# Optimization experiments

Measured on AMD Instinct MI355X. Metric: run time of the kernel, lower is better.

Reference implementation:

```python
import math
import jax, jax.numpy as jnp
import numpy as np

D_MODEL = 1024
N_HEADS = 16
D_K = D_MODEL // N_HEADS


def _alibi_slopes(n_heads):
    # Faithful to the torch _get_slopes: slopes[i] = 2**(-8 + i), subsampled if
    # n_heads is not a power of two.
    power = 2 ** math.ceil(math.log2(n_heads))
    slopes = np.array([2.0 ** (-8 + i) for i in range(power)], dtype=np.float32)
    if n_heads != power:
        ratio = power // n_heads
        slopes = slopes[np.arange(0, power, ratio)][:n_heads]
    return jnp.asarray(slopes)


def setup_inputs() -> dict:
    key = jax.random.key(0)
    ks = jax.random.split(key, 11)
    B, S, D = 2, 2048, D_MODEL
    w = 0.02  # weight init scale
    return {
        "query": jax.random.normal(ks[0], (B, S, D), jnp.float32),
        "key": jax.random.normal(ks[1], (B, S, D), jnp.float32),
        "value": jax.random.normal(ks[2], (B, S, D), jnp.float32),
        "Wq": jax.random.normal(ks[3], (D, D), jnp.float32) * w,
        "bq": jax.random.normal(ks[4], (D,), jnp.float32) * w,
        "Wk": jax.random.normal(ks[5], (D, D), jnp.float32) * w,
        "bk": jax.random.normal(ks[6], (D,), jnp.float32) * w,
        "Wv": jax.random.normal(ks[7], (D, D), jnp.float32) * w,
        "bv": jax.random.normal(ks[8], (D,), jnp.float32) * w,
        "Wo": jax.random.normal(ks[9], (D, D), jnp.float32) * w,
        "bo": jax.random.normal(ks[10], (D,), jnp.float32) * w,
    }


def reference(query, key, value, Wq, bq, Wk, bk, Wv, bv, Wo, bo):
    B, Sq, D = query.shape
    Sk = key.shape[1]
    H, dk = N_HEADS, D_K

    # projections (torch Linear: x @ W.T + b)
    q = (query @ Wq.T + bq).reshape(B, Sq, H, dk).transpose(0, 2, 1, 3)  # [B,H,Sq,dk]
    k = (key @ Wk.T + bk).reshape(B, Sk, H, dk).transpose(0, 2, 1, 3)    # [B,H,Sk,dk]
    v = (value @ Wv.T + bv).reshape(B, Sk, H, dk).transpose(0, 2, 1, 3)  # [B,H,Sk,dk]

    scores = jnp.einsum("bhqd,bhkd->bhqk", q, k) / jnp.sqrt(jnp.float32(dk))

    # ALiBi bias: slopes[h] * (i - j), non-causal path (is_causal=False)
    dist = (jnp.arange(Sq)[:, None] - jnp.arange(Sk)[None, :]).astype(scores.dtype)
    slopes = _alibi_slopes(H)
    scores = scores + slopes[None, :, None, None] * dist[None, None, :, :]

    attn = jax.nn.softmax(scores, axis=-1)
    out = jnp.einsum("bhqk,bhkd->bhqd", attn, v)          # [B,H,Sq,dk]
    out = out.transpose(0, 2, 1, 3).reshape(B, Sq, D)     # [B,Sq,D]
    return out @ Wo.T + bo
```

## Files before the change

### kernel.cpp

```cpp
#include <hip/hip_runtime.h>

typedef __bf16 bf16_t;
typedef bf16_t bf16x8 __attribute__((ext_vector_type(8)));
typedef float f32x4 __attribute__((ext_vector_type(4)));
typedef float f32x16 __attribute__((ext_vector_type(16)));
typedef unsigned short u16x4 __attribute__((ext_vector_type(4)));
typedef unsigned int u32x4v __attribute__((ext_vector_type(4)));
typedef unsigned int u32;

#define DEV static __device__ __forceinline__


DEV unsigned short f2bf(float f) {
  unsigned int u = __builtin_bit_cast(unsigned int, f);
  u = (u + 0x7fffu + ((u >> 16) & 1u)) >> 16;
  return (unsigned short)u;
}

DEV float fexp2(float x) {
  float r;
  asm("v_exp_f32 %0, %1" : "=v"(r) : "v"(x));
  return r;
}

DEV u32 cvtpk(float lo, float hi_) {
  u32 r;
  asm("v_cvt_pk_bf16_f32 %0, %1, %2" : "=v"(r) : "v"(lo), "v"(hi_));
  return r;
}

DEV void plswap(u32& a, u32& b) {
  asm("v_permlane32_swap_b32 %0, %1" : "+v"(a), "+v"(b));
}

DEV void async_ld16(const unsigned short* gsrc, unsigned short* lbase, int lane) {
#if __has_builtin(__builtin_amdgcn_global_load_lds)
  __builtin_amdgcn_global_load_lds(
      (const __attribute__((address_space(1))) unsigned int*)(const void*)gsrc,
      (__attribute__((address_space(3))) unsigned int*)(void*)lbase, 16, 0, 0);
#else
  *reinterpret_cast<u32x4v*>(reinterpret_cast<char*>(lbase) + lane * 16) =
      *reinterpret_cast<const u32x4v*>(gsrc);
#endif
}


DEV void cvt_body(const float* __restrict__ src, unsigned short* __restrict__ dst, int i) {
  const float4* s = reinterpret_cast<const float4*>(src) + (size_t)i * 2;
  float4 a = s[0], c = s[1];
  u16x4 lo = {f2bf(a.x), f2bf(a.y), f2bf(a.z), f2bf(a.w)};
  u16x4 hi = {f2bf(c.x), f2bf(c.y), f2bf(c.z), f2bf(c.w)};
  u16x4* d = reinterpret_cast<u16x4*>(dst) + (size_t)i * 2;
  d[0] = lo;
  d[1] = hi;
}

__global__ __launch_bounds__(256) void cvt_all(
    const float* __restrict__ q, const float* __restrict__ k, const float* __restrict__ v,
    const float* __restrict__ Wq, const float* __restrict__ Wk, const float* __restrict__ Wv,
    const float* __restrict__ Wo, unsigned short* dq, unsigned short* dk, unsigned short* dv,
    unsigned short* dWq, unsigned short* dWk, unsigned short* dWv, unsigned short* dWo) {
  const int bid = blockIdx.x;
  const float* src;
  unsigned short* dst;
  int i;
  if (bid < 6144) {
    const int z = bid >> 11;
    src = z == 0 ? q : z == 1 ? k : v;
    dst = z == 0 ? dq : z == 1 ? dk : dv;
    i = (bid & 2047) * 256 + threadIdx.x;
  } else {
    const int z = (bid - 6144) >> 9;
    src = z == 0 ? Wq : z == 1 ? Wk : z == 2 ? Wv : Wo;
    dst = z == 0 ? dWq : z == 1 ? dWk : z == 2 ? dWv : dWo;
    i = ((bid - 6144) & 511) * 256 + threadIdx.x;
  }
  cvt_body(src, dst, i);
}


DEV void stage_a128(const unsigned short* __restrict__ G, int row0, int k0,
                    unsigned short* lbuf, int lane, int wv) {
#pragma unroll
  for (int r = 0; r < 4; ++r) {
    const int rowA = (r * 4 + wv) * 8 + (lane >> 3);
    const int chunk = (lane & 7) ^ (rowA & 7);
    async_ld16(G + (size_t)(row0 + rowA) * 1024 + k0 + chunk * 8, lbuf + (r * 4 + wv) * 512,
               lane);
  }
}

DEV void stage_b64(const unsigned short* __restrict__ G, int row0, int k0,
                   unsigned short* lbuf, int lane, int wv) {
#pragma unroll
  for (int r = 0; r < 2; ++r) {
    const int rowB = (r * 4 + wv) * 8 + (lane >> 3);
    const int chunk = (lane & 7) ^ (rowB & 7);
    async_ld16(G + (size_t)(row0 + rowB) * 1024 + k0 + chunk * 8, lbuf + (r * 4 + wv) * 512,
               lane);
  }
}

DEV void gemm_core(const unsigned short* __restrict__ X, const unsigned short* __restrict__ W,
                   unsigned short* lA0, unsigned short* lA1, unsigned short* lB0,
                   unsigned short* lB1, int bm0, int bn0, int lane, int wv, int wm, int wn,
                   f32x4 acc[4][2]) {
  stage_a128(X, bm0, 0, lA0, lane, wv);
  stage_b64(W, bn0, 0, lB0, lane, wv);
  __syncthreads();
  for (int kt = 0; kt < 16; ++kt) {
    unsigned short* lA = (kt & 1) ? lA1 : lA0;
    unsigned short* lB = (kt & 1) ? lB1 : lB0;
    unsigned short* nA = (kt & 1) ? lA0 : lA1;
    unsigned short* nB = (kt & 1) ? lB0 : lB1;
    if (kt < 15) {
      stage_a128(X, bm0, (kt + 1) * 64, nA, lane, wv);
      stage_b64(W, bn0, (kt + 1) * 64, nB, lane, wv);
    }
#pragma unroll
    for (int kk = 0; kk < 2; ++kk) {
      bf16x8 af[4], bfr[2];
#pragma unroll
      for (int f = 0; f < 4; ++f) {
        const int rowA = wm * 64 + f * 16 + (lane & 15);
        const int cA = (kk * 4 + (lane >> 4)) ^ (rowA & 7);
        af[f] = *reinterpret_cast<const bf16x8*>(lA + rowA * 64 + cA * 8);
      }
#pragma unroll
      for (int f = 0; f < 2; ++f) {
        const int rowB = wn * 32 + f * 16 + (lane & 15);
        const int cB = (kk * 4 + (lane >> 4)) ^ (rowB & 7);
        bfr[f] = *reinterpret_cast<const bf16x8*>(lB + rowB * 64 + cB * 8);
      }
#pragma unroll
      for (int i = 0; i < 4; ++i)
#pragma unroll
        for (int j = 0; j < 2; ++j)
          acc[i][j] = __builtin_amdgcn_mfma_f32_16x16x32_bf16(af[i], bfr[j], acc[i][j], 0, 0, 0);
    }
    __syncthreads();
  }
}


__global__ __launch_bounds__(256, 3) void gemm_qkv_kernel(
    const unsigned short* __restrict__ Xq, const unsigned short* __restrict__ Xk,
    const unsigned short* __restrict__ Xv, const unsigned short* __restrict__ Wq,
    const unsigned short* __restrict__ Wk, const unsigned short* __restrict__ Wv,
    const float* __restrict__ bq, const float* __restrict__ bk, const float* __restrict__ bv,
    unsigned short* __restrict__ Qp, unsigned short* __restrict__ Kp,
    unsigned short* __restrict__ Vp, unsigned* __restrict__ nb2) {
  __shared__ unsigned short lA[2][8192];
  __shared__ unsigned short lB[2][4096];
  const int flat = blockIdx.x + 32 * blockIdx.y + 512 * blockIdx.z;
  const int swz = (flat & 7) * 192 + (flat >> 3);
  const int bx = swz & 31;
  const int by = (swz >> 5) & 15;
  const int bz = swz >> 9;
  const unsigned short* X;
  const unsigned short* W;
  const float* bias;
  unsigned short* dst;
  if (bz == 0) { X = Xq; W = Wq; bias = bq; dst = Qp; }
  else if (bz == 1) { X = Xk; W = Wk; bias = bk; dst = Kp; }
  else { X = Xv; W = Wv; bias = bv; dst = Vp; }
  const bool zV = (bz == 2);
  const bool zK = (bz == 1) && (nb2 != nullptr);
  const int lane = threadIdx.x & 63, wv = threadIdx.x >> 6;
  const int wm = wv >> 1, wn = wv & 1;
  const int bm0 = bx * 128, bn0 = by * 64;
  f32x4 acc[4][2] = {};
  gemm_core(X, W, lA[0], lA[1], lB[0], lB[1], bm0, bn0, lane, wv, wm, wn, acc);
  float rowmax = 0.0f;
#pragma unroll
  for (int i = 0; i < 4; ++i) {
    const int mbase = bm0 + wm * 64 + i * 16 + ((lane >> 4) << 2);
#pragma unroll
    for (int r = 0; r < 4; ++r) {
      const int m = mbase + r;
      const int b = m >> 11, s = m & 2047;
      float ssp = 0.0f;
#pragma unroll
      for (int j = 0; j < 2; ++j) {
        const int n = bn0 + wn * 32 + j * 16 + (lane & 15);
        const float val = acc[i][j][r] + bias[n];
        const unsigned short v16 = f2bf(val);
        const int h = n >> 6, d = n & 63;
        if (zV)
          dst[((size_t)(b * 16 + h) * 64 + d) * 2048 + s] = v16;
        else
          dst[((size_t)(b * 16 + h) * 2048 + s) * 64 + d] = v16;
        ssp = __builtin_fmaf(val, val, ssp);
      }
      if (zK) {
        ssp += __shfl_xor(ssp, 1);
        ssp += __shfl_xor(ssp, 2);
        ssp += __shfl_xor(ssp, 4);
        ssp += __shfl_xor(ssp, 8);
        rowmax = fmaxf(rowmax, ssp);
      }
    }
  }
  if (zK) {
    rowmax = fmaxf(rowmax, __shfl_xor(rowmax, 16));
    rowmax = fmaxf(rowmax, __shfl_xor(rowmax, 32));
    if (lane == 0)
      atomicMax(nb2 + (((bm0 >> 11) * 16 + by) * 2 + wn), __float_as_uint(rowmax));
  }
}


__global__ __launch_bounds__(256, 3) void gemm_out_kernel(const unsigned short* __restrict__ X,
                                                          const unsigned short* __restrict__ W,
                                                          const float* __restrict__ bias,
                                                          float* __restrict__ out) {
  __shared__ unsigned short lA[2][8192];
  __shared__ unsigned short lB[2][4096];
  const int flat = blockIdx.x + 32 * blockIdx.y;
  const int swz = (flat & 7) * 64 + (flat >> 3);
  const int bx = swz & 31, by = swz >> 5;
  const int lane = threadIdx.x & 63, wv = threadIdx.x >> 6;
  const int wm = wv >> 1, wn = wv & 1;
  const int bm0 = bx * 128, bn0 = by * 64;
  f32x4 acc[4][2] = {};
  gemm_core(X, W, lA[0], lA[1], lB[0], lB[1], bm0, bn0, lane, wv, wm, wn, acc);
#pragma unroll
  for (int i = 0; i < 4; ++i) {
    const int mbase = bm0 + wm * 64 + i * 16 + ((lane >> 4) << 2);
#pragma unroll
    for (int j = 0; j < 2; ++j) {
      const int n = bn0 + wn * 32 + j * 16 + (lane & 15);
      const float bia = bias[n];
#pragma unroll
      for (int r = 0; r < 4; ++r) out[(size_t)(mbase + r) * 1024 + n] = acc[i][j][r] + bia;
    }
  }
}


__global__ __launch_bounds__(256) void knorm_kernel(const unsigned short* __restrict__ Kp,
                                                    unsigned* __restrict__ nb2) {
  const int bh = blockIdx.y;
  const int s = blockIdx.x * 256 + threadIdx.x;
  const u32x4v* row = reinterpret_cast<const u32x4v*>(Kp + ((size_t)bh * 2048 + s) * 64);
  float ss0 = 0.0f, ss1 = 0.0f;
#pragma unroll
  for (int c = 0; c < 8; ++c) {
    u32x4v u = row[c];
    float acc = 0.0f;
#pragma unroll
    for (int e = 0; e < 4; ++e) {
      const float lo = __builtin_bit_cast(float, u[e] << 16);
      const float hi = __builtin_bit_cast(float, u[e] & 0xFFFF0000u);
      acc = __builtin_fmaf(lo, lo, acc);
      acc = __builtin_fmaf(hi, hi, acc);
    }
    if (c < 4) ss0 += acc;
    else ss1 += acc;
  }
#pragma unroll
  for (int off = 1; off <= 32; off <<= 1) {
    ss0 = fmaxf(ss0, __shfl_xor(ss0, off));
    ss1 = fmaxf(ss1, __shfl_xor(ss1, off));
  }
  if ((threadIdx.x & 63) == 0) {
    atomicMax(nb2 + bh * 2, __float_as_uint(ss0));
    atomicMax(nb2 + bh * 2 + 1, __float_as_uint(ss1));
  }
}


__global__ __launch_bounds__(128) void attn_prepass(const unsigned short* __restrict__ Qp,
                                                    const unsigned short* __restrict__ Kp,
                                                    const unsigned* __restrict__ nb2,
                                                    float* __restrict__ mfA,
                                                    float* __restrict__ bltA) {
  __shared__ float sred[4];
  const int lane = threadIdx.x & 63, wv = threadIdx.x >> 6;
  const int lq = lane & 31, hi = lane >> 5;
  const int qt = blockIdx.x, bh = blockIdx.y, h = bh & 15;
  const float L2E = 1.4426950408889634f;
  const float slope2 = ldexpf(L2E, h - 8);
  const float SC2 = 0.125f * L2E;
  const size_t headoff = (size_t)bh * 2048 * 64;
  const unsigned short* Qh = Qp + headoff;
  const unsigned short* Kh = Kp + headoff;
  const int q_glob = qt * 64 + wv * 32 + lq;

  bf16x8 qf[4];
#pragma unroll
  for (int tt = 0; tt < 4; ++tt)
    qf[tt] = *reinterpret_cast<const bf16x8*>(Qh + (size_t)q_glob * 64 + tt * 16 + hi * 8);

  float qq = 0.0f;
#pragma unroll
  for (int tt = 0; tt < 4; ++tt)
#pragma unroll
    for (int e = 0; e < 8; ++e) {
      const float x = (float)qf[tt][e];
      qq = __builtin_fmaf(x, x, qq);
    }
  qq += __shfl_xor(qq, 32);
#pragma unroll
  for (int off = 1; off <= 16; off <<= 1) qq = fmaxf(qq, __shfl_xor(qq, off));

  f32x16 s0 = {}, s1 = {};
#pragma unroll
  for (int tt = 0; tt < 4; ++tt) {
    bf16x8 k0 = *reinterpret_cast<const bf16x8*>(Kh + (size_t)lq * 64 + tt * 16 + hi * 8);
    s0 = __builtin_amdgcn_mfma_f32_32x32x16_bf16(k0, qf[tt], s0, 0, 0, 0);
    bf16x8 k1 = *reinterpret_cast<const bf16x8*>(Kh + (size_t)(32 + lq) * 64 + tt * 16 + hi * 8);
    s1 = __builtin_amdgcn_mfma_f32_32x32x16_bf16(k1, qf[tt], s1, 0, 0, 0);
  }
  float zmax = -3.0e38f;
#pragma unroll
  for (int r = 0; r < 16; ++r) {
    const float cb = -slope2 * (float)(4 * hi + (r & 3) + 8 * (r >> 2));
    const float x0 = __builtin_fmaf(s0[r], SC2, cb);
    const float x1 = __builtin_fmaf(s1[r], SC2, cb - slope2 * 32.0f);
    zmax = fmaxf(zmax, fmaxf(x0, x1));
  }
  zmax = fmaxf(zmax, __shfl_xor(zmax, 32));
  float zmin = zmax;
#pragma unroll
  for (int off = 1; off <= 16; off <<= 1) zmin = fminf(zmin, __shfl_xor(zmin, off));
  if (lane == 0) {
    sred[wv] = zmin;
    sred[2 + wv] = qq;
  }
  __syncthreads();
  if (threadIdx.x == 0) {
    const float mf = fminf(sred[0], sred[1]);
    const float qn = sqrtf(fmaxf(sred[2], sred[3]));
    const float nk2 = __uint_as_float(nb2[bh * 2]) + __uint_as_float(nb2[bh * 2 + 1]);
    const float nk = sqrtf(nk2);
    mfA[bh * 32 + qt] = mf;
    bltA[bh * 32 + qt] = qn * nk * SC2;
  }
}


DEV void stage_tile64(const unsigned short* __restrict__ Gbase, size_t stride, int colbase,
                      unsigned short* lbuf, int lane, int wv) {
#pragma unroll
  for (int i = 0; i < 4; ++i) {
    const int r = i * 16 + wv * 8 + (lane >> 3);
    const int chunk = (lane & 7) ^ (r & 7);
    async_ld16(Gbase + (size_t)r * stride + colbase + chunk * 8, lbuf + (i * 16 + wv * 8) * 64,
               lane);
  }
}

__global__ __launch_bounds__(128) void attn_split_kernel(
    const unsigned short* __restrict__ Qp, const unsigned short* __restrict__ Kp,
    const unsigned short* __restrict__ VTp, const float* __restrict__ mfA,
    const float* __restrict__ bltA, float* __restrict__ ML, float* __restrict__ Opart, int Ct,
    int nsplit) {
  __shared__ unsigned short Kb[2][64 * 64];
  __shared__ unsigned short Vb[2][64 * 64];
  const int lane = threadIdx.x & 63, wv = threadIdx.x >> 6;
  const int lq = lane & 31, hi = lane >> 5;
  const int qt = blockIdx.x, sp = blockIdx.y, bh = blockIdx.z;
  const int h = bh & 15;
  const int idx = bh * 32 + qt;
  const float L2E = 1.4426950408889634f;
  const float slope2 = ldexpf(L2E, h - 8);
  const float SC2 = 0.125f * L2E;
  const float m_floor = mfA[idx], blt = bltA[idx];
  const float tf = (blt - m_floor + 34.0f) / (slope2 * 64.0f);
  const int T_act = min(32, (int)tf + 1);
  const int t0 = sp * Ct;
  const int nt = min(Ct, T_act - t0);
  float* mlb = ML + ((size_t)idx * nsplit + sp) * 128;
  if (nt <= 0) {
    mlb[threadIdx.x] = threadIdx.x < 64 ? -3.0e38f : 0.0f;
    return;
  }
  float* ob = Opart + ((size_t)idx * nsplit + sp) * 4096;
  const size_t headoff = (size_t)bh * 2048 * 64;
  const unsigned short* Qh = Qp + headoff;
  const unsigned short* Kh = Kp + headoff;
  const unsigned short* VTh = VTp + headoff;
  const int q_glob = qt * 64 + wv * 32 + lq;

  float cb0[16], cb1[16];
#pragma unroll
  for (int r = 0; r < 16; ++r) {
    cb0[r] = -slope2 * (float)(4 * hi + (r & 3) + 8 * (r >> 2));
    cb1[r] = cb0[r] - slope2 * 32.0f;
  }

  bf16x8 qf[4];
#pragma unroll
  for (int tt = 0; tt < 4; ++tt)
    qf[tt] = *reinterpret_cast<const bf16x8*>(Qh + (size_t)q_glob * 64 + tt * 16 + hi * 8);

  stage_tile64(Kh + (size_t)(t0 * 64) * 64, 64, 0, Kb[0], lane, wv);
  stage_tile64(VTh, 2048, t0 * 64, Vb[0], lane, wv);
  __syncthreads();

  f32x16 acc0 = {}, acc1 = {};
  float m_run = m_floor, l_run = 0.0f;

  for (int ti = 0; ti < nt; ++ti) {
    const int kv0 = (t0 + ti) * 64;
    const float s2k = slope2 * (float)kv0;
    const unsigned short* Kc = Kb[ti & 1];
    const unsigned short* Vc = Vb[ti & 1];
    if (ti + 1 < nt) {
      stage_tile64(Kh + (size_t)(kv0 + 64) * 64, 64, 0, Kb[(ti + 1) & 1], lane, wv);
      stage_tile64(VTh, 2048, kv0 + 64, Vb[(ti + 1) & 1], lane, wv);
    }
    f32x16 s0 = {}, s1 = {};
    __builtin_amdgcn_s_setprio(1);
#pragma unroll
    for (int tt = 0; tt < 4; ++tt) {
      {
        const int row = lq;
        const int ch = (tt * 2 + hi) ^ (row & 7);
        bf16x8 kf = *reinterpret_cast<const bf16x8*>(Kc + row * 64 + ch * 8);
        s0 = __builtin_amdgcn_mfma_f32_32x32x16_bf16(kf, qf[tt], s0, 0, 0, 0);
      }
      {
        const int row = 32 + lq;
        const int ch = (tt * 2 + hi) ^ (row & 7);
        bf16x8 kf = *reinterpret_cast<const bf16x8*>(Kc + row * 64 + ch * 8);
        s1 = __builtin_amdgcn_mfma_f32_32x32x16_bf16(kf, qf[tt], s1, 0, 0, 0);
      }
    }
    __builtin_amdgcn_s_setprio(0);
    float zmax = -3.0e38f;
#pragma unroll
    for (int r = 0; r < 16; ++r) {
      s0[r] = __builtin_fmaf(s0[r], SC2, cb0[r]);
      s1[r] = __builtin_fmaf(s1[r], SC2, cb1[r]);
      zmax = fmaxf(zmax, fmaxf(s0[r], s1[r]));
    }
    zmax = fmaxf(zmax, __shfl_xor(zmax, 32));
    const float tmax_true = zmax - s2k;
    if (__any(tmax_true > m_run + 8.0f)) {
      const float m_new = fmaxf(m_run, tmax_true);
      const float alpha = fexp2(m_run - m_new);
      m_run = m_new;
      l_run *= alpha;
      acc0 *= alpha;
      acc1 *= alpha;
    }
    const float mm = m_run + s2k;
    float ps0 = 0.0f, ps1 = 0.0f;
#pragma unroll
    for (int r = 0; r < 16; ++r) {
      const float p0 = fexp2(s0[r] - mm);
      const float p1 = fexp2(s1[r] - mm);
      s0[r] = p0;
      s1[r] = p1;
      ps0 += p0;
      ps1 += p1;
    }
    float psum = ps0 + ps1;
    psum += __shfl_xor(psum, 32);
    l_run += psum;
    bf16x8 pf[4];
#pragma unroll
    for (int half = 0; half < 2; ++half) {
      u32 w0 = cvtpk(s0[half * 8 + 0], s0[half * 8 + 1]);
      u32 w2 = cvtpk(s0[half * 8 + 4], s0[half * 8 + 5]);
      plswap(w0, w2);
      u32 w1 = cvtpk(s0[half * 8 + 2], s0[half * 8 + 3]);
      u32 w3 = cvtpk(s0[half * 8 + 6], s0[half * 8 + 7]);
      plswap(w1, w3);
      u32x4v ww = {w0, w1, w2, w3};
      pf[half] = __builtin_bit_cast(bf16x8, ww);
    }
#pragma unroll
    for (int half = 0; half < 2; ++half) {
      u32 w0 = cvtpk(s1[half * 8 + 0], s1[half * 8 + 1]);
      u32 w2 = cvtpk(s1[half * 8 + 4], s1[half * 8 + 5]);
      plswap(w0, w2);
      u32 w1 = cvtpk(s1[half * 8 + 2], s1[half * 8 + 3]);
      u32 w3 = cvtpk(s1[half * 8 + 6], s1[half * 8 + 7]);
      plswap(w1, w3);
      u32x4v ww = {w0, w1, w2, w3};
      pf[2 + half] = __builtin_bit_cast(bf16x8, ww);
    }
    __builtin_amdgcn_s_setprio(1);
#pragma unroll
    for (int tt = 0; tt < 4; ++tt) {
      {
        const int row = lq;
        const int ch = (tt * 2 + hi) ^ (row & 7);
        bf16x8 vf = *reinterpret_cast<const bf16x8*>(Vc + row * 64 + ch * 8);
        acc0 = __builtin_amdgcn_mfma_f32_32x32x16_bf16(vf, pf[tt], acc0, 0, 0, 0);
      }
      {
        const int row = 32 + lq;
        const int ch = (tt * 2 + hi) ^ (row & 7);
        bf16x8 vf = *reinterpret_cast<const bf16x8*>(Vc + row * 64 + ch * 8);
        acc1 = __builtin_amdgcn_mfma_f32_32x32x16_bf16(vf, pf[tt], acc1, 0, 0, 0);
      }
    }
    __builtin_amdgcn_s_setprio(0);
    __syncthreads();
  }
  const int qloc = wv * 32 + lq;
  if (hi == 0) {
    mlb[qloc] = m_run;
    mlb[64 + qloc] = l_run;
  }
#pragma unroll
  for (int g = 0; g < 4; ++g) {
    f32x4 w0, w1;
#pragma unroll
    for (int e = 0; e < 4; ++e) {
      w0[e] = acc0[g * 4 + e];
      w1[e] = acc1[g * 4 + e];
    }
    *reinterpret_cast<f32x4*>(ob + qloc * 64 + g * 8 + 4 * hi) = w0;
    *reinterpret_cast<f32x4*>(ob + qloc * 64 + 32 + g * 8 + 4 * hi) = w1;
  }
}


__global__ __launch_bounds__(256) void attn_combine(const float* __restrict__ ML,
                                                    const float* __restrict__ Opart,
                                                    unsigned short* __restrict__ Ob, int nsplit) {
  const int idx = blockIdx.x;
  const int bh = idx >> 5, qt = idx & 31;
  const int h = bh & 15, b = bh >> 4;
  const int q = threadIdx.x >> 2, d0 = (threadIdx.x & 3) * 16;
  const float* mlb = ML + (size_t)idx * nsplit * 128;
  const float* ob = Opart + (size_t)idx * nsplit * 4096;
  float m_g = -3.0e38f;
  for (int s = 0; s < nsplit; ++s) m_g = fmaxf(m_g, mlb[s * 128 + q]);
  float l = 0.0f;
  f32x4 acc[4] = {};
  for (int s = 0; s < nsplit; ++s) {
    const float ms = mlb[s * 128 + q], ls = mlb[s * 128 + 64 + q];
    const float w = fexp2(ms - m_g);
    const float wl = w * ls;
    if (wl > 0.0f) {
      l += wl;
      const f32x4* src = reinterpret_cast<const f32x4*>(ob + (size_t)s * 4096 + q * 64 + d0);
#pragma unroll
      for (int j = 0; j < 4; ++j) {
        f32x4 v = src[j];
#pragma unroll
        for (int e = 0; e < 4; ++e) acc[j][e] = __builtin_fmaf(w, v[e], acc[j][e]);
      }
    }
  }
  const float invl = 1.0f / l;
  unsigned short* orow = Ob + ((size_t)(b * 2048 + qt * 64 + q)) * 1024 + h * 64 + d0;
#pragma unroll
  for (int j = 0; j < 4; ++j) {
    u16x4 pk;
#pragma unroll
    for (int e = 0; e < 4; ++e) pk[e] = f2bf(acc[j][e] * invl);
    *reinterpret_cast<u16x4*>(orow + j * 4) = pk;
  }
}


extern "C" void kernel_launch(void* const* d_in, const int* in_sizes, int n_in, void* d_out,
                              int out_size, void* d_ws, size_t ws_size, hipStream_t stream) {
  const float* q = (const float*)d_in[0];
  const float* k = (const float*)d_in[1];
  const float* v = (const float*)d_in[2];
  const float* Wq = (const float*)d_in[3];
  const float* bq = (const float*)d_in[4];
  const float* Wk = (const float*)d_in[5];
  const float* bk = (const float*)d_in[6];
  const float* Wv = (const float*)d_in[7];
  const float* bv = (const float*)d_in[8];
  const float* Wo = (const float*)d_in[9];
  const float* bo = (const float*)d_in[10];

  char* ws = (char*)d_ws;
  const size_t MB = 1024 * 1024;
  unsigned short* qb = (unsigned short*)(ws + 0 * MB);
  unsigned short* kb = (unsigned short*)(ws + 8 * MB);
  unsigned short* vb = (unsigned short*)(ws + 16 * MB);
  unsigned short* Wqb = (unsigned short*)(ws + 24 * MB);
  unsigned short* Wkb = (unsigned short*)(ws + 26 * MB);
  unsigned short* Wvb = (unsigned short*)(ws + 28 * MB);
  unsigned short* Wob = (unsigned short*)(ws + 30 * MB);
  unsigned short* Qp = (unsigned short*)(ws + 32 * MB);
  unsigned short* Kp = (unsigned short*)(ws + 40 * MB);
  unsigned short* VTp = (unsigned short*)(ws + 48 * MB);
  unsigned short* Obf = (unsigned short*)(ws + 0 * MB);

  int nsplit;
  float *mfA, *bltA, *ML, *Opart;
  unsigned* nb2;
  bool fold_knorm;
  if (ws_size >= (size_t)121 * MB) nsplit = 4;
  else if (ws_size >= (size_t)89 * MB) nsplit = 2;
  else nsplit = 1;
  if (ws_size >= (size_t)73 * MB) {
    fold_knorm = true;
    nb2 = (unsigned*)(ws + 56 * MB);
    mfA = (float*)(ws + 24 * MB + 4096);
    bltA = (float*)(ws + 24 * MB + 8192);
    ML = (float*)(ws + 26 * MB);
    Opart = (float*)(ws + 56 * MB + 4096);
  } else {
    fold_knorm = false;
    nsplit = 1;
    nb2 = (unsigned*)(ws + 26 * MB);
    mfA = (float*)(ws + 26 * MB + 4096);
    bltA = (float*)(ws + 26 * MB + 8192);
    ML = (float*)(ws + 26 * MB + 65536);
    Opart = (float*)(ws + 8 * MB);
  }
  const int Ct = 32 / nsplit;

  cvt_all<<<8192, 256, 0, stream>>>(q, k, v, Wq, Wk, Wv, Wo, qb, kb, vb, Wqb, Wkb, Wvb, Wob);
  hipMemsetAsync(nb2, 0, 64 * sizeof(unsigned), stream);
  gemm_qkv_kernel<<<dim3(32, 16, 3), 256, 0, stream>>>(qb, kb, vb, Wqb, Wkb, Wvb, bq, bk, bv, Qp,
                                                       Kp, VTp, fold_knorm ? nb2 : nullptr);
  if (!fold_knorm) knorm_kernel<<<dim3(8, 32), 256, 0, stream>>>(Kp, nb2);
  attn_prepass<<<dim3(32, 32), 128, 0, stream>>>(Qp, Kp, nb2, mfA, bltA);
  attn_split_kernel<<<dim3(32, nsplit, 32), 128, 0, stream>>>(Qp, Kp, VTp, mfA, bltA, ML, Opart,
                                                              Ct, nsplit);
  attn_combine<<<1024, 256, 0, stream>>>(ML, Opart, Obf, nsplit);
  gemm_out_kernel<<<dim3(32, 16), 256, 0, stream>>>(Obf, Wob, bo, (float*)d_out);
}
```

Measured before the change: 131.9 us.

## Enlarge projection GEMM tiles to 128x128 and drop block swizzle

Both projection GEMMs now use 128x128 output tiles, with each wave computing a 64x64 sub-tile (4x4 MFMA accumulators) instead of 128x64. This halves the number of blocks and raises reuse of each staged LDS fragment. The L2-friendly block swizzle and the occupancy hint in launch_bounds are removed. Because a head's 64 columns now fall under a single wave, the key-norm bookkeeping collapses from two partial maxima per head to one. The costs are more registers and LDS per block, fewer blocks to fill the CUs, and loss of the swizzled L2 locality.

```diff
diff --git a/kernel.cpp b/kernel.cpp
--- a/kernel.cpp
+++ b/kernel.cpp
@@ -79,21 +79,10 @@
 }
 
 
-DEV void stage_a128(const unsigned short* __restrict__ G, int row0, int k0,
+DEV void stage_b128(const unsigned short* __restrict__ G, int row0, int k0,
                     unsigned short* lbuf, int lane, int wv) {
 #pragma unroll
   for (int r = 0; r < 4; ++r) {
-    const int rowA = (r * 4 + wv) * 8 + (lane >> 3);
-    const int chunk = (lane & 7) ^ (rowA & 7);
-    async_ld16(G + (size_t)(row0 + rowA) * 1024 + k0 + chunk * 8, lbuf + (r * 4 + wv) * 512,
-               lane);
-  }
-}
-
-DEV void stage_b64(const unsigned short* __restrict__ G, int row0, int k0,
-                   unsigned short* lbuf, int lane, int wv) {
-#pragma unroll
-  for (int r = 0; r < 2; ++r) {
     const int rowB = (r * 4 + wv) * 8 + (lane >> 3);
     const int chunk = (lane & 7) ^ (rowB & 7);
     async_ld16(G + (size_t)(row0 + rowB) * 1024 + k0 + chunk * 8, lbuf + (r * 4 + wv) * 512,
@@ -101,12 +90,34 @@
   }
 }
 
+DEV void mfma_step(const unsigned short* lA, const unsigned short* lB, int lane, int wm, int wn,
+                   f32x4 acc[4][4]) {
+#pragma unroll
+  for (int kk = 0; kk < 2; ++kk) {
+    bf16x8 af[4], bfr[4];
+#pragma unroll
+    for (int f = 0; f < 4; ++f) {
+      const int rowA = wm * 64 + f * 16 + (lane & 15);
+      const int cA = (kk * 4 + (lane >> 4)) ^ (rowA & 7);
+      af[f] = *reinterpret_cast<const bf16x8*>(lA + rowA * 64 + cA * 8);
+      const int rowB = wn * 64 + f * 16 + (lane & 15);
+      const int cB = (kk * 4 + (lane >> 4)) ^ (rowB & 7);
+      bfr[f] = *reinterpret_cast<const bf16x8*>(lB + rowB * 64 + cB * 8);
+    }
+#pragma unroll
+    for (int i = 0; i < 4; ++i)
+#pragma unroll
+      for (int j = 0; j < 4; ++j)
+        acc[i][j] = __builtin_amdgcn_mfma_f32_16x16x32_bf16(af[i], bfr[j], acc[i][j], 0, 0, 0);
+  }
+}
+
 DEV void gemm_core(const unsigned short* __restrict__ X, const unsigned short* __restrict__ W,
                    unsigned short* lA0, unsigned short* lA1, unsigned short* lB0,
                    unsigned short* lB1, int bm0, int bn0, int lane, int wv, int wm, int wn,
-                   f32x4 acc[4][2]) {
-  stage_a128(X, bm0, 0, lA0, lane, wv);
-  stage_b64(W, bn0, 0, lB0, lane, wv);
+                   f32x4 acc[4][4]) {
+  stage_b128(X, bm0, 0, lA0, lane, wv);
+  stage_b128(W, bn0, 0, lB0, lane, wv);
   __syncthreads();
   for (int kt = 0; kt < 16; ++kt) {
     unsigned short* lA = (kt & 1) ? lA1 : lA0;
@@ -114,36 +125,16 @@
     unsigned short* nA = (kt & 1) ? lA0 : lA1;
     unsigned short* nB = (kt & 1) ? lB0 : lB1;
     if (kt < 15) {
-      stage_a128(X, bm0, (kt + 1) * 64, nA, lane, wv);
-      stage_b64(W, bn0, (kt + 1) * 64, nB, lane, wv);
-    }
-#pragma unroll
-    for (int kk = 0; kk < 2; ++kk) {
-      bf16x8 af[4], bfr[2];
-#pragma unroll
-      for (int f = 0; f < 4; ++f) {
-        const int rowA = wm * 64 + f * 16 + (lane & 15);
-        const int cA = (kk * 4 + (lane >> 4)) ^ (rowA & 7);
-        af[f] = *reinterpret_cast<const bf16x8*>(lA + rowA * 64 + cA * 8);
-      }
-#pragma unroll
-      for (int f = 0; f < 2; ++f) {
-        const int rowB = wn * 32 + f * 16 + (lane & 15);
-        const int cB = (kk * 4 + (lane >> 4)) ^ (rowB & 7);
-        bfr[f] = *reinterpret_cast<const bf16x8*>(lB + rowB * 64 + cB * 8);
-      }
-#pragma unroll
-      for (int i = 0; i < 4; ++i)
-#pragma unroll
-        for (int j = 0; j < 2; ++j)
-          acc[i][j] = __builtin_amdgcn_mfma_f32_16x16x32_bf16(af[i], bfr[j], acc[i][j], 0, 0, 0);
-    }
+      stage_b128(X, bm0, (kt + 1) * 64, nA, lane, wv);
+      stage_b128(W, bn0, (kt + 1) * 64, nB, lane, wv);
+    }
+    mfma_step(lA, lB, lane, wm, wn, acc);
     __syncthreads();
   }
 }
 
 
-__global__ __launch_bounds__(256, 3) void gemm_qkv_kernel(
+__global__ __launch_bounds__(256) void gemm_qkv_kernel(
     const unsigned short* __restrict__ Xq, const unsigned short* __restrict__ Xk,
     const unsigned short* __restrict__ Xv, const unsigned short* __restrict__ Wq,
     const unsigned short* __restrict__ Wk, const unsigned short* __restrict__ Wv,
@@ -151,25 +142,20 @@
     unsigned short* __restrict__ Qp, unsigned short* __restrict__ Kp,
     unsigned short* __restrict__ Vp, unsigned* __restrict__ nb2) {
   __shared__ unsigned short lA[2][8192];
-  __shared__ unsigned short lB[2][4096];
-  const int flat = blockIdx.x + 32 * blockIdx.y + 512 * blockIdx.z;
-  const int swz = (flat & 7) * 192 + (flat >> 3);
-  const int bx = swz & 31;
-  const int by = (swz >> 5) & 15;
-  const int bz = swz >> 9;
+  __shared__ unsigned short lB[2][8192];
   const unsigned short* X;
   const unsigned short* W;
   const float* bias;
   unsigned short* dst;
-  if (bz == 0) { X = Xq; W = Wq; bias = bq; dst = Qp; }
-  else if (bz == 1) { X = Xk; W = Wk; bias = bk; dst = Kp; }
+  if (blockIdx.z == 0) { X = Xq; W = Wq; bias = bq; dst = Qp; }
+  else if (blockIdx.z == 1) { X = Xk; W = Wk; bias = bk; dst = Kp; }
   else { X = Xv; W = Wv; bias = bv; dst = Vp; }
-  const bool zV = (bz == 2);
-  const bool zK = (bz == 1) && (nb2 != nullptr);
+  const bool zV = (blockIdx.z == 2);
+  const bool zK = (blockIdx.z == 1) && (nb2 != nullptr);
   const int lane = threadIdx.x & 63, wv = threadIdx.x >> 6;
   const int wm = wv >> 1, wn = wv & 1;
-  const int bm0 = bx * 128, bn0 = by * 64;
-  f32x4 acc[4][2] = {};
+  const int bm0 = blockIdx.x * 128, bn0 = blockIdx.y * 128;
+  f32x4 acc[4][4] = {};
   gemm_core(X, W, lA[0], lA[1], lB[0], lB[1], bm0, bn0, lane, wv, wm, wn, acc);
   float rowmax = 0.0f;
 #pragma unroll
@@ -181,8 +167,8 @@
       const int b = m >> 11, s = m & 2047;
       float ssp = 0.0f;
 #pragma unroll
-      for (int j = 0; j < 2; ++j) {
-        const int n = bn0 + wn * 32 + j * 16 + (lane & 15);
+      for (int j = 0; j < 4; ++j) {
+        const int n = bn0 + wn * 64 + j * 16 + (lane & 15);
         const float val = acc[i][j][r] + bias[n];
         const unsigned short v16 = f2bf(val);
         const int h = n >> 6, d = n & 63;
@@ -204,32 +190,31 @@
   if (zK) {
     rowmax = fmaxf(rowmax, __shfl_xor(rowmax, 16));
     rowmax = fmaxf(rowmax, __shfl_xor(rowmax, 32));
-    if (lane == 0)
-      atomicMax(nb2 + (((bm0 >> 11) * 16 + by) * 2 + wn), __float_as_uint(rowmax));
-  }
-}
-
-
-__global__ __launch_bounds__(256, 3) void gemm_out_kernel(const unsigned short* __restrict__ X,
-                                                          const unsigned short* __restrict__ W,
-                                                          const float* __restrict__ bias,
-                                                          float* __restrict__ out) {
+    if (lane == 0) {
+      const int bh = (bm0 >> 11) * 16 + blockIdx.y * 2 + wn;
+      atomicMax(nb2 + bh, __float_as_uint(rowmax));
+    }
+  }
+}
+
+
+__global__ __launch_bounds__(256) void gemm_out_kernel(const unsigned short* __restrict__ X,
+                                                       const unsigned short* __restrict__ W,
+                                                       const float* __restrict__ bias,
+                                                       float* __restrict__ out) {
   __shared__ unsigned short lA[2][8192];
-  __shared__ unsigned short lB[2][4096];
-  const int flat = blockIdx.x + 32 * blockIdx.y;
-  const int swz = (flat & 7) * 64 + (flat >> 3);
-  const int bx = swz & 31, by = swz >> 5;
+  __shared__ unsigned short lB[2][8192];
   const int lane = threadIdx.x & 63, wv = threadIdx.x >> 6;
   const int wm = wv >> 1, wn = wv & 1;
-  const int bm0 = bx * 128, bn0 = by * 64;
-  f32x4 acc[4][2] = {};
+  const int bm0 = blockIdx.x * 128, bn0 = blockIdx.y * 128;
+  f32x4 acc[4][4] = {};
   gemm_core(X, W, lA[0], lA[1], lB[0], lB[1], bm0, bn0, lane, wv, wm, wn, acc);
 #pragma unroll
   for (int i = 0; i < 4; ++i) {
     const int mbase = bm0 + wm * 64 + i * 16 + ((lane >> 4) << 2);
 #pragma unroll
-    for (int j = 0; j < 2; ++j) {
-      const int n = bn0 + wn * 32 + j * 16 + (lane & 15);
+    for (int j = 0; j < 4; ++j) {
+      const int n = bn0 + wn * 64 + j * 16 + (lane & 15);
       const float bia = bias[n];
 #pragma unroll
       for (int r = 0; r < 4; ++r) out[(size_t)(mbase + r) * 1024 + n] = acc[i][j][r] + bia;
@@ -243,30 +228,21 @@
   const int bh = blockIdx.y;
   const int s = blockIdx.x * 256 + threadIdx.x;
   const u32x4v* row = reinterpret_cast<const u32x4v*>(Kp + ((size_t)bh * 2048 + s) * 64);
-  float ss0 = 0.0f, ss1 = 0.0f;
+  float ss = 0.0f;
 #pragma unroll
   for (int c = 0; c < 8; ++c) {
     u32x4v u = row[c];
-    float acc = 0.0f;
 #pragma unroll
     for (int e = 0; e < 4; ++e) {
       const float lo = __builtin_bit_cast(float, u[e] << 16);
       const float hi = __builtin_bit_cast(float, u[e] & 0xFFFF0000u);
-      acc = __builtin_fmaf(lo, lo, acc);
-      acc = __builtin_fmaf(hi, hi, acc);
-    }
-    if (c < 4) ss0 += acc;
-    else ss1 += acc;
-  }
-#pragma unroll
-  for (int off = 1; off <= 32; off <<= 1) {
-    ss0 = fmaxf(ss0, __shfl_xor(ss0, off));
-    ss1 = fmaxf(ss1, __shfl_xor(ss1, off));
-  }
-  if ((threadIdx.x & 63) == 0) {
-    atomicMax(nb2 + bh * 2, __float_as_uint(ss0));
-    atomicMax(nb2 + bh * 2 + 1, __float_as_uint(ss1));
-  }
+      ss = __builtin_fmaf(lo, lo, ss);
+      ss = __builtin_fmaf(hi, hi, ss);
+    }
+  }
+#pragma unroll
+  for (int off = 1; off <= 32; off <<= 1) ss = fmaxf(ss, __shfl_xor(ss, off));
+  if ((threadIdx.x & 63) == 0) atomicMax(nb2 + bh, __float_as_uint(ss));
 }
 
 
@@ -332,8 +308,7 @@
   if (threadIdx.x == 0) {
     const float mf = fminf(sred[0], sred[1]);
     const float qn = sqrtf(fmaxf(sred[2], sred[3]));
-    const float nk2 = __uint_as_float(nb2[bh * 2]) + __uint_as_float(nb2[bh * 2 + 1]);
-    const float nk = sqrtf(nk2);
+    const float nk = sqrtf(__uint_as_float(nb2[bh]));
     mfA[bh * 32 + qt] = mf;
     bltA[bh * 32 + qt] = qn * nk * SC2;
   }
@@ -601,7 +576,7 @@
     nb2 = (unsigned*)(ws + 56 * MB);
     mfA = (float*)(ws + 24 * MB + 4096);
     bltA = (float*)(ws + 24 * MB + 8192);
-    ML = (float*)(ws + 26 * MB);
+    ML = (float*)(ws + 26 * MB + 65536);
     Opart = (float*)(ws + 56 * MB + 4096);
   } else {
     fold_knorm = false;
@@ -616,12 +591,12 @@
 
   cvt_all<<<8192, 256, 0, stream>>>(q, k, v, Wq, Wk, Wv, Wo, qb, kb, vb, Wqb, Wkb, Wvb, Wob);
   hipMemsetAsync(nb2, 0, 64 * sizeof(unsigned), stream);
-  gemm_qkv_kernel<<<dim3(32, 16, 3), 256, 0, stream>>>(qb, kb, vb, Wqb, Wkb, Wvb, bq, bk, bv, Qp,
-                                                       Kp, VTp, fold_knorm ? nb2 : nullptr);
+  gemm_qkv_kernel<<<dim3(32, 8, 3), 256, 0, stream>>>(qb, kb, vb, Wqb, Wkb, Wvb, bq, bk, bv, Qp,
+                                                      Kp, VTp, fold_knorm ? nb2 : nullptr);
   if (!fold_knorm) knorm_kernel<<<dim3(8, 32), 256, 0, stream>>>(Kp, nb2);
   attn_prepass<<<dim3(32, 32), 128, 0, stream>>>(Qp, Kp, nb2, mfA, bltA);
   attn_split_kernel<<<dim3(32, nsplit, 32), 128, 0, stream>>>(Qp, Kp, VTp, mfA, bltA, ML, Opart,
                                                               Ct, nsplit);
   attn_combine<<<1024, 256, 0, stream>>>(ML, Opart, Obf, nsplit);
-  gemm_out_kernel<<<dim3(32, 16), 256, 0, stream>>>(Obf, Wob, bo, (float*)d_out);
-}
+  gemm_out_kernel<<<dim3(32, 8), 256, 0, stream>>>(Obf, Wob, bo, (float*)d_out);
+}
```

New measurement: 124.6 us. 1.06x faster.
